# Optimization experiments

Measured on AMD Instinct MI355X. Metric: run time of the kernel, lower is better.

## Reference

```python
import jax, jax.numpy as jnp
import numpy as np

H, W = 72, 128            # raster_h, raster_w
THICK = 0.03              # raster_thickness
SHARP = 80.0              # sigmoid sharpness
NRS = 64                  # match_resample_n
BIG = 1e9                 # finite stand-in for inf (grad-safe)
PTS_W, TAN_W, CURV_W, OVL_W = 5.0, 1.0, 0.5, 2.0


def _grid_xy():
    ys = jnp.linspace(0.0, 1.0, H)
    xs = jnp.linspace(0.0, 1.0, W)
    yy, xx = jnp.meshgrid(ys, xs, indexing='ij')
    return jnp.stack([xx, yy], -1).reshape(-1, 2)  # [H*W, 2]


def _prepare_mask(vis):
    # visibility -> per-point mask; curves with <2 visible points fall back to all-visible
    raw = vis > 0.5
    fallback = raw.sum(-1) < 2
    return jnp.where(fallback[:, None], 1.0, raw.astype(jnp.float32))  # [m, p]


def _resample(curves, pm, num):
    # arc-length resampling of [m, p, 2] polylines to [m, num, 2]
    m, p, _ = curves.shape
    seg_valid = pm[:, :-1] * pm[:, 1:]
    seg_len = jnp.linalg.norm(curves[:, 1:] - curves[:, :-1], axis=-1) * seg_valid
    cum = jnp.concatenate([jnp.zeros((m, 1), curves.dtype), jnp.cumsum(seg_len, -1)], -1)  # [m, p]
    total = cum[:, -1]
    base_t = jnp.linspace(0.0, 1.0, num)
    t = base_t[None] * total[:, None]  # [m, num]
    idx = jax.vmap(lambda c, tt: jnp.searchsorted(c, tt, side='right'))(cum, t) - 1
    idx = jnp.clip(idx, 0, p - 2)
    left = jnp.take_along_axis(curves[:, :-1], idx[..., None], axis=1)
    right = jnp.take_along_axis(curves[:, 1:], idx[..., None], axis=1)
    lt = jnp.take_along_axis(cum[:, :-1], idx, axis=1)
    rt = jnp.take_along_axis(cum[:, 1:], idx, axis=1)
    alpha = ((t - lt) / jnp.maximum(rt - lt, 1e-8))[..., None]
    out = left + alpha * (right - left)
    return jnp.where((total < 1e-8)[:, None, None], curves[:, :1, :], out)


def _tangents(pts):
    # central-difference unit tangents, [m, n, 2]
    fwd = jnp.concatenate([pts[:, 1:2] - pts[:, 0:1],
                           pts[:, 2:] - pts[:, :-2],
                           pts[:, -1:] - pts[:, -2:-1]], axis=1)
    return fwd / jnp.maximum(jnp.linalg.norm(fwd, axis=-1, keepdims=True), 1e-8)


def _pt2poly(A, B):
    # mean over resampled points of A of min point-to-segment distance to polyline B
    # A: [qa, r, 2], B: [qb, r, 2] -> [qa, qb]
    seg_a = B[:, :-1]
    ab = B[:, 1:] - seg_a
    denom = jnp.maximum((ab * ab).sum(-1), 1e-8)  # [qb, s]
    ap = A[:, None, :, None, :] - seg_a[None, :, None]           # [qa, qb, r, s, 2]
    t = jnp.clip((ap * ab[None, :, None]).sum(-1) / denom[None, :, None], 0.0, 1.0)
    proj = seg_a[None, :, None] + t[..., None] * ab[None, :, None]
    dist = jnp.linalg.norm(A[:, None, :, None, :] - proj, axis=-1)  # [qa, qb, r, s]
    return dist.min(-1).mean(-1)


def _smooth_l1(x, y):
    d = jnp.abs(x - y)
    return jnp.where(d < 1.0, 0.5 * d * d, d - 0.5)


def _soft_mask(curves, pm, grid):
    # soft rasterization of polylines: [m, p, 2] -> [m, H*W]
    seg_a = curves[:, :-1]
    ab = curves[:, 1:] - seg_a
    denom = jnp.maximum((ab * ab).sum(-1), 1e-8)          # [m, s]
    seg_valid = (pm[:, :-1] * pm[:, 1:]) > 0.5
    ap = grid[None, :, None, :] - seg_a[:, None]          # [m, HW, s, 2]
    t = jnp.clip((ap * ab[:, None]).sum(-1) / denom[:, None], 0.0, 1.0)
    proj = seg_a[:, None] + t[..., None] * ab[:, None]
    dist = jnp.linalg.norm(grid[None, :, None, :] - proj, axis=-1)  # [m, HW, s]
    dist = jnp.where(seg_valid[:, None], dist, BIG)
    min_dist = dist.min(-1)
    # fallback to nearest visible point when a curve has no valid segment
    no_valid = ~seg_valid.any(-1)
    pd = jnp.linalg.norm(grid[None, :, None, :] - curves[:, None], axis=-1)  # [m, HW, p]
    pd = jnp.where(pm[:, None] > 0.5, pd, BIG)
    min_dist = jnp.where(no_valid[:, None], pd.min(-1), min_dist)
    return jax.nn.sigmoid((THICK - min_dist) * SHARP)


def _cost_single(pred, gtp, gtv, grid):
    gt_pm = _prepare_mask(gtv)
    ones_pm = jnp.ones(pred.shape[:2], pred.dtype)
    pred_rs = _resample(pred, ones_pm, NRS)
    gt_rs = _resample(gtp, gt_pm, NRS)
    d_pg = _pt2poly(pred_rs, gt_rs)
    d_gp = _pt2poly(gt_rs, pred_rs).T
    sym = 0.5 * (d_pg + d_gp)                                   # [Q, M]
    pt = _tangents(pred_rs)
    gt_t = _tangents(gt_rs)
    tan = 1.0 - jnp.abs((pt[:, None] * gt_t[None]).sum(-1)).mean(-1)
    ps = pred_rs[:, 2:] - 2 * pred_rs[:, 1:-1] + pred_rs[:, :-2]
    gs = gt_rs[:, 2:] - 2 * gt_rs[:, 1:-1] + gt_rs[:, :-2]
    curv = _smooth_l1(ps[:, None], gs[None]).mean((-1, -2))
    pmask = _soft_mask(pred, ones_pm, grid)                     # [Q, HW]
    gmask = _soft_mask(gtp, gt_pm, grid)                        # [M, HW]
    inter = jnp.minimum(pmask[:, None], gmask[None]).sum(-1)
    union = jnp.maximum(pmask[:, None], gmask[None]).sum(-1)
    overlap = 1.0 - inter / (union + 1e-8)
    return PTS_W * sym + TAN_W * tan + CURV_W * curv + OVL_W * overlap


def setup_inputs() -> dict:
    key = jax.random.key(0)
    k1, k2, k3, k4 = jax.random.split(key, 4)
    return {
        'pred_pts': jax.random.uniform(k1, (2, 40, 24, 2), jnp.float32),
        'gt_pts': jax.random.uniform(k2, (2, 24, 24, 2), jnp.float32),
        'gt_vis': jax.random.uniform(k3, (2, 24, 24), jnp.float32),
        'gt_exist': jax.random.uniform(k4, (2, 24), jnp.float32),
    }


def reference(pred_pts, gt_pts, gt_vis, gt_exist):
    grid = _grid_xy()
    cost = jax.vmap(lambda p, g, v: _cost_single(p, g, v, grid))(pred_pts, gt_pts, gt_vis)
    # zero out columns for non-existent GT lanes (original skips them via boolean indexing)
    return cost * (gt_exist > 0.5).astype(cost.dtype)[:, None, :]  # [B, Q, M]
```

## Files before the change

### kernel.cpp

```cpp
#include <hip/hip_runtime.h>
#include <math.h>

#define Hh 72
#define Ww 128
#define HW (Hh*Ww)
#define NP 24
#define NSEG (NP-1)
#define Mp 40
#define Ng 24
#define Bb 2
#define NRS 64
#define THICKc 0.03f
#define SHARPc 80.0f
#define NCURV (Bb*(Mp+Ng))

__global__ __launch_bounds__(64) void k_prep(
    const float* __restrict__ pred,
    const float* __restrict__ gt,
    const float* __restrict__ vis,
    float* __restrict__ predRS,
    float* __restrict__ gtRS,
    float* __restrict__ segData,
    int*   __restrict__ segCount)
{
    int c = blockIdx.x;
    bool isPred = (c < Bb * Mp);
    int b   = isPred ? (c / Mp) : ((c - Bb * Mp) / Ng);
    int idx = isPred ? (c % Mp) : ((c - Bb * Mp) % Ng);
    const float* src = isPred ? pred + (size_t)(b * Mp + idx) * NP * 2
                              : gt   + (size_t)(b * Ng + idx) * NP * 2;
    int tid = threadIdx.x;

    __shared__ float qx[NP], qy[NP], pm[NP], cum[NP];
    __shared__ int   sidx[NP];
    __shared__ int   s_mode;
    __shared__ float s_total;

    if (tid < NP) {
        float2 v = ((const float2*)src)[tid];
        qx[tid] = v.x; qy[tid] = v.y;
        pm[tid] = isPred ? 1.0f
                         : ((vis[(b * Ng + idx) * NP + tid] > 0.5f) ? 1.0f : 0.0f);
    }
    __syncthreads();
    if (tid == 0) {
        if (!isPred) {
            float s = 0.0f;
            for (int p = 0; p < NP; p++) s += pm[p];
            if (s < 2.0f)
                for (int p = 0; p < NP; p++) pm[p] = 1.0f;
        }
        float acc = 0.0f;
        cum[0] = 0.0f;
        for (int s = 0; s < NSEG; s++) {
            float dx = qx[s + 1] - qx[s], dy = qy[s + 1] - qy[s];
            acc += sqrtf(dx * dx + dy * dy) * (pm[s] * pm[s + 1]);
            cum[s + 1] = acc;
        }
        s_total = acc;
        int n = 0;
        for (int s = 0; s < NSEG; s++) sidx[s] = (pm[s] * pm[s + 1] > 0.5f) ? n++ : -1;
        if (n > 0) {
            s_mode = 0;
        } else {
            s_mode = 1;
            for (int p = 0; p < NP; p++) sidx[p] = (pm[p] > 0.5f) ? n++ : -1;
        }
        segCount[c] = n;
    }
    __syncthreads();

    if (s_mode == 0) {
        if (tid < NSEG && sidx[tid] >= 0) {
            float ax = qx[tid], ay = qy[tid];
            float abx = qx[tid + 1] - ax, aby = qy[tid + 1] - ay;
            float inv = 1.0f / fmaxf(abx * abx + aby * aby, 1e-8f);
            float* r = segData + ((size_t)c * NP + sidx[tid]) * 8;
            r[0] = ax;  r[1] = ay;  r[2] = abx;       r[3] = aby;
            r[4] = abx * inv; r[5] = aby * inv; r[6] = (ax * abx + ay * aby) * inv; r[7] = 0.f;
        }
    } else {
        if (tid < NP && sidx[tid] >= 0) {
            float* r = segData + ((size_t)c * NP + sidx[tid]) * 8;
            r[0] = qx[tid]; r[1] = qy[tid]; r[2] = 0.f; r[3] = 0.f;
            r[4] = 0.f;     r[5] = 0.f;     r[6] = 0.f; r[7] = 0.f;
        }
    }

    float total = s_total;
    float t = ((float)tid / 63.0f) * total;
    int cnt = 0;
    for (int p = 0; p < NP; p++) cnt += (cum[p] <= t) ? 1 : 0;
    int id2 = cnt - 1;
    id2 = (id2 < 0) ? 0 : ((id2 > NP - 2) ? NP - 2 : id2);
    float lt = cum[id2], rt = cum[id2 + 1];
    float alpha = (t - lt) / fmaxf(rt - lt, 1e-8f);
    float ox = qx[id2] + alpha * (qx[id2 + 1] - qx[id2]);
    float oy = qy[id2] + alpha * (qy[id2 + 1] - qy[id2]);
    if (total < 1e-8f) { ox = qx[0]; oy = qy[0]; }
    float* dst = isPred ? predRS + ((size_t)(b * Mp + idx) * NRS + tid) * 2
                        : gtRS   + ((size_t)(b * Ng + idx) * NRS + tid) * 2;
    dst[0] = ox; dst[1] = oy;
}

__global__ __launch_bounds__(256) void k_softmask(
    const float* __restrict__ segData,
    const int*   __restrict__ segCount,
    float* __restrict__ maskAll)
{
    int c = blockIdx.y;
    int g = blockIdx.x * 256 + threadIdx.x;
    int n = segCount[c];
    const float4* sd = (const float4*)(segData + (size_t)c * NP * 8);

    float gx = (float)(g & (Ww - 1)) * (1.0f / 127.0f);
    float gy = (float)(g >> 7)       * (1.0f / 71.0f);

    float best2 = 1e30f;
    for (int s = 0; s < n; s++) {
        float4 A  = sd[s * 2];
        float4 Bv = sd[s * 2 + 1];
        float t = fmaf(gx, Bv.x, fmaf(gy, Bv.y, -Bv.z));
        t = fminf(fmaxf(t, 0.0f), 1.0f);
        float dx = gx - fmaf(t, A.z, A.x);
        float dy = gy - fmaf(t, A.w, A.y);
        best2 = fminf(best2, fmaf(dx, dx, dy * dy));
    }
    float mind = sqrtf(best2);
    float mval = 1.0f / (1.0f + __expf((mind - THICKc) * SHARPc));
    maskAll[(size_t)c * HW + g] = mval;
}

__global__ __launch_bounds__(256) void k_cost(
    const float* __restrict__ predRS,
    const float* __restrict__ gtRS,
    const float* __restrict__ maskAll,
    const float* __restrict__ gtExist,
    float* __restrict__ out)
{
    int blk = blockIdx.x;
    int tj = blk % 12;
    int ti = (blk / 12) % 20;
    int b  = blk / (12 * 20);
    int i0 = ti * 2, j0 = tj * 2;
    int tid = threadIdx.x;
    int lane = tid & 63, w = tid >> 6;

    __shared__ float sPx[2][NRS], sPy[2][NRS], sGx[2][NRS], sGy[2][NRS];
    __shared__ float partA[4][8];
    __shared__ float cham[4][3];

    {
        int ci = tid >> 6, pt = tid & 63;
        if (ci < 2) {
            float2 v = ((const float2*)predRS)[(b * Mp + i0 + ci) * NRS + pt];
            sPx[ci][pt] = v.x; sPy[ci][pt] = v.y;
        } else {
            int cj = ci - 2;
            float2 v = ((const float2*)gtRS)[(b * Ng + j0 + cj) * NRS + pt];
            sGx[cj][pt] = v.x; sGy[cj][pt] = v.y;
        }
    }
    __syncthreads();

    const float4* P0 = (const float4*)(maskAll + (size_t)(b * Mp + i0)     * HW);
    const float4* P1 = (const float4*)(maskAll + (size_t)(b * Mp + i0 + 1) * HW);
    const float4* Q0 = (const float4*)(maskAll + (size_t)(Bb * Mp + b * Ng + j0)     * HW);
    const float4* Q1 = (const float4*)(maskAll + (size_t)(Bb * Mp + b * Ng + j0 + 1) * HW);
    float sm00 = 0, sm01 = 0, sm10 = 0, sm11 = 0;
    float sp0 = 0, sp1 = 0, sq0 = 0, sq1 = 0;
    for (int g = tid; g < HW / 4; g += 256) {
        float4 p0 = P0[g], p1 = P1[g], q0 = Q0[g], q1 = Q1[g];
        sp0 += p0.x + p0.y + p0.z + p0.w;
        sp1 += p1.x + p1.y + p1.z + p1.w;
        sq0 += q0.x + q0.y + q0.z + q0.w;
        sq1 += q1.x + q1.y + q1.z + q1.w;
        sm00 += fminf(p0.x,q0.x) + fminf(p0.y,q0.y) + fminf(p0.z,q0.z) + fminf(p0.w,q0.w);
        sm01 += fminf(p0.x,q1.x) + fminf(p0.y,q1.y) + fminf(p0.z,q1.z) + fminf(p0.w,q1.w);
        sm10 += fminf(p1.x,q0.x) + fminf(p1.y,q0.y) + fminf(p1.z,q0.z) + fminf(p1.w,q0.w);
        sm11 += fminf(p1.x,q1.x) + fminf(p1.y,q1.y) + fminf(p1.z,q1.z) + fminf(p1.w,q1.w);
    }
    for (int off = 32; off > 0; off >>= 1) {
        sm00 += __shfl_down(sm00, off); sm01 += __shfl_down(sm01, off);
        sm10 += __shfl_down(sm10, off); sm11 += __shfl_down(sm11, off);
        sp0  += __shfl_down(sp0,  off); sp1  += __shfl_down(sp1,  off);
        sq0  += __shfl_down(sq0,  off); sq1  += __shfl_down(sq1,  off);
    }
    if (lane == 0) {
        partA[w][0] = sm00; partA[w][1] = sm01; partA[w][2] = sm10; partA[w][3] = sm11;
        partA[w][4] = sp0;  partA[w][5] = sp1;  partA[w][6] = sq0;  partA[w][7] = sq1;
    }

    {
        int a = w >> 1, cj = w & 1;
        const float* PX = sPx[a];  const float* PY = sPy[a];
        const float* GX = sGx[cj]; const float* GY = sGy[cj];
        float p0x = PX[lane], p0y = PY[lane];
        float q0x = GX[lane], q0y = GY[lane];
        float b1 = 1e30f, b2 = 1e30f;
        for (int s = 0; s < NRS - 1; s++) {
            {
                float ax = GX[s], ay = GY[s];
                float abx = GX[s + 1] - ax, aby = GY[s + 1] - ay;
                float denom = fmaxf(abx * abx + aby * aby, 1e-8f);
                float t = ((p0x - ax) * abx + (p0y - ay) * aby) / denom;
                t = fminf(fmaxf(t, 0.0f), 1.0f);
                float dx = p0x - (ax + t * abx), dy = p0y - (ay + t * aby);
                b1 = fminf(b1, dx * dx + dy * dy);
            }
            {
                float ax = PX[s], ay = PY[s];
                float abx = PX[s + 1] - ax, aby = PY[s + 1] - ay;
                float denom = fmaxf(abx * abx + aby * aby, 1e-8f);
                float t = ((q0x - ax) * abx + (q0y - ay) * aby) / denom;
                t = fminf(fmaxf(t, 0.0f), 1.0f);
                float dx = q0x - (ax + t * abx), dy = q0y - (ay + t * aby);
                b2 = fminf(b2, dx * dx + dy * dy);
            }
        }
        float symv = 0.5f * (sqrtf(b1) + sqrtf(b2));

        int kp = (lane == NRS - 1) ? NRS - 1 : lane + 1;
        int km = (lane == 0) ? 0 : lane - 1;
        float tx = PX[kp] - PX[km], ty = PY[kp] - PY[km];
        float nrm = fmaxf(sqrtf(tx * tx + ty * ty), 1e-8f);
        tx /= nrm; ty /= nrm;
        float gtx = GX[kp] - GX[km], gty = GY[kp] - GY[km];
        float nrm2 = fmaxf(sqrtf(gtx * gtx + gty * gty), 1e-8f);
        gtx /= nrm2; gty /= nrm2;
        float tanv = fabsf(tx * gtx + ty * gty);

        float curvv = 0.0f;
        if (lane < NRS - 2) {
            float psx = PX[lane + 2] - 2.0f * PX[lane + 1] + PX[lane];
            float psy = PY[lane + 2] - 2.0f * PY[lane + 1] + PY[lane];
            float gsx = GX[lane + 2] - 2.0f * GX[lane + 1] + GX[lane];
            float gsy = GY[lane + 2] - 2.0f * GY[lane + 1] + GY[lane];
            float d1 = fabsf(psx - gsx);
            float d2 = fabsf(psy - gsy);
            float c1 = (d1 < 1.0f) ? 0.5f * d1 * d1 : d1 - 0.5f;
            float c2 = (d2 < 1.0f) ? 0.5f * d2 * d2 : d2 - 0.5f;
            curvv = c1 + c2;
        }
        for (int off = 32; off > 0; off >>= 1) {
            symv  += __shfl_down(symv,  off);
            tanv  += __shfl_down(tanv,  off);
            curvv += __shfl_down(curvv, off);
        }
        if (lane == 0) { cham[w][0] = symv; cham[w][1] = tanv; cham[w][2] = curvv; }
    }
    __syncthreads();

    if (tid < 4) {
        int a2 = tid >> 1, c2 = tid & 1;
        float Smin = partA[0][tid] + partA[1][tid] + partA[2][tid] + partA[3][tid];
        float Sp = partA[0][4 + a2] + partA[1][4 + a2] + partA[2][4 + a2] + partA[3][4 + a2];
        float Sq = partA[0][6 + c2] + partA[1][6 + c2] + partA[2][6 + c2] + partA[3][6 + c2];
        float Smax = Sp + Sq - Smin;
        float overlap = 1.0f - Smin / (Smax + 1e-8f);
        float sym  = cham[tid][0] * (1.0f / 64.0f);
        float tanl = 1.0f - cham[tid][1] * (1.0f / 64.0f);
        float curv = cham[tid][2] * (1.0f / 124.0f);
        float cost = 5.0f * sym + 1.0f * tanl + 0.5f * curv + 2.0f * overlap;
        float e = (gtExist[b * Ng + j0 + c2] > 0.5f) ? 1.0f : 0.0f;
        out[(size_t)(b * Mp + i0 + a2) * Ng + j0 + c2] = cost * e;
    }
}

extern "C" void kernel_launch(void* const* d_in, const int* in_sizes, int n_in,
                              void* d_out, int out_size, void* d_ws, size_t ws_size,
                              hipStream_t stream) {
    (void)in_sizes; (void)n_in; (void)out_size; (void)ws_size;
    const float* pred  = (const float*)d_in[0];
    const float* gt    = (const float*)d_in[1];
    const float* vis   = (const float*)d_in[2];
    const float* exist = (const float*)d_in[3];

    float* ws      = (float*)d_ws;
    float* predRS  = ws;
    float* gtRS    = predRS + (size_t)Bb * Mp * NRS * 2;
    float* segData = gtRS   + (size_t)Bb * Ng * NRS * 2;
    int*   segCount= (int*)(segData + (size_t)NCURV * NP * 8);
    float* maskAll = (float*)(segCount + 128);
    float* outp    = (float*)d_out;

    hipLaunchKernelGGL(k_prep, dim3(NCURV), dim3(64), 0, stream,
                       pred, gt, vis, predRS, gtRS, segData, segCount);
    hipLaunchKernelGGL(k_softmask, dim3(HW / 256, NCURV), dim3(256), 0, stream,
                       segData, segCount, maskAll);
    hipLaunchKernelGGL(k_cost, dim3(Bb * 20 * 12), dim3(256), 0, stream,
                       predRS, gtRS, maskAll, exist, outp);
}
```

Baseline: 100.8 us.

## Fuse three kernels into one cooperative kernel with grid-wide syncs

Merges the prep, soft-mask and cost kernels into a single cooperative launch of 480 blocks, with grid.sync barriers between the phases. The soft-mask phase becomes a grid-stride loop over curve and pixel-chunk tasks. The aim is to remove the launch gaps between three kernels. The cost is grid-barrier overhead, a fixed block count that must stay co-resident, and reduced parallelism in the mask phase.

Measured after the change: 312.9 us. 3.11x slower.

```diff
diff --git a/kernel.cpp b/kernel.cpp
--- a/kernel.cpp
+++ b/kernel.cpp
@@ -1,5 +1,8 @@
 #include <hip/hip_runtime.h>
+#include <hip/hip_cooperative_groups.h>
 #include <math.h>
+
+namespace cg = cooperative_groups;
 
 #define Hh 72
 #define Ww 128
@@ -13,22 +16,22 @@
 #define THICKc 0.03f
 #define SHARPc 80.0f
 #define NCURV (Bb*(Mp+Ng))
-
-__global__ __launch_bounds__(64) void k_prep(
+#define NBLK 480
+#define NCHUNK (HW/256)
+
+__global__ __launch_bounds__(256) void k_fused(
     const float* __restrict__ pred,
     const float* __restrict__ gt,
     const float* __restrict__ vis,
+    const float* __restrict__ gtExist,
     float* __restrict__ predRS,
     float* __restrict__ gtRS,
     float* __restrict__ segData,
-    int*   __restrict__ segCount)
+    int*   __restrict__ segCount,
+    float* __restrict__ maskAll,
+    float* __restrict__ out)
 {
-    int c = blockIdx.x;
-    bool isPred = (c < Bb * Mp);
-    int b   = isPred ? (c / Mp) : ((c - Bb * Mp) / Ng);
-    int idx = isPred ? (c % Mp) : ((c - Bb * Mp) % Ng);
-    const float* src = isPred ? pred + (size_t)(b * Mp + idx) * NP * 2
-                              : gt   + (size_t)(b * Ng + idx) * NP * 2;
+    cg::grid_group grid = cg::this_grid();
     int tid = threadIdx.x;
 
     __shared__ float qx[NP], qy[NP], pm[NP], cum[NP];
@@ -36,234 +39,237 @@
     __shared__ int   s_mode;
     __shared__ float s_total;
 
-    if (tid < NP) {
-        float2 v = ((const float2*)src)[tid];
-        qx[tid] = v.x; qy[tid] = v.y;
-        pm[tid] = isPred ? 1.0f
-                         : ((vis[(b * Ng + idx) * NP + tid] > 0.5f) ? 1.0f : 0.0f);
+    if (blockIdx.x < NCURV) {
+        int c = blockIdx.x;
+        bool isPred = (c < Bb * Mp);
+        int b   = isPred ? (c / Mp) : ((c - Bb * Mp) / Ng);
+        int idx = isPred ? (c % Mp) : ((c - Bb * Mp) % Ng);
+        const float* src = isPred ? pred + (size_t)(b * Mp + idx) * NP * 2
+                                  : gt   + (size_t)(b * Ng + idx) * NP * 2;
+        if (tid < NP) {
+            float2 v = ((const float2*)src)[tid];
+            qx[tid] = v.x; qy[tid] = v.y;
+            pm[tid] = isPred ? 1.0f
+                             : ((vis[(b * Ng + idx) * NP + tid] > 0.5f) ? 1.0f : 0.0f);
+        }
+        __syncthreads();
+        if (tid == 0) {
+            if (!isPred) {
+                float s = 0.0f;
+                for (int p = 0; p < NP; p++) s += pm[p];
+                if (s < 2.0f)
+                    for (int p = 0; p < NP; p++) pm[p] = 1.0f;
+            }
+            float acc = 0.0f;
+            cum[0] = 0.0f;
+            for (int s = 0; s < NSEG; s++) {
+                float dx = qx[s + 1] - qx[s], dy = qy[s + 1] - qy[s];
+                acc += sqrtf(dx * dx + dy * dy) * (pm[s] * pm[s + 1]);
+                cum[s + 1] = acc;
+            }
+            s_total = acc;
+            int n = 0;
+            for (int s = 0; s < NSEG; s++) sidx[s] = (pm[s] * pm[s + 1] > 0.5f) ? n++ : -1;
+            if (n > 0) {
+                s_mode = 0;
+            } else {
+                s_mode = 1;
+                for (int p = 0; p < NP; p++) sidx[p] = (pm[p] > 0.5f) ? n++ : -1;
+            }
+            segCount[c] = n;
+        }
+        __syncthreads();
+
+        if (s_mode == 0) {
+            if (tid < NSEG && sidx[tid] >= 0) {
+                float ax = qx[tid], ay = qy[tid];
+                float abx = qx[tid + 1] - ax, aby = qy[tid + 1] - ay;
+                float inv = 1.0f / fmaxf(abx * abx + aby * aby, 1e-8f);
+                float* r = segData + ((size_t)c * NP + sidx[tid]) * 8;
+                r[0] = ax;        r[1] = ay;        r[2] = abx; r[3] = aby;
+                r[4] = abx * inv; r[5] = aby * inv;
+                r[6] = (ax * abx + ay * aby) * inv; r[7] = 0.f;
+            }
+        } else {
+            if (tid < NP && sidx[tid] >= 0) {
+                float* r = segData + ((size_t)c * NP + sidx[tid]) * 8;
+                r[0] = qx[tid]; r[1] = qy[tid]; r[2] = 0.f; r[3] = 0.f;
+                r[4] = 0.f;     r[5] = 0.f;     r[6] = 0.f; r[7] = 0.f;
+            }
+        }
+
+        if (tid < NRS) {
+            float total = s_total;
+            float t = ((float)tid / 63.0f) * total;
+            int cnt = 0;
+            for (int p = 0; p < NP; p++) cnt += (cum[p] <= t) ? 1 : 0;
+            int id2 = cnt - 1;
+            id2 = (id2 < 0) ? 0 : ((id2 > NP - 2) ? NP - 2 : id2);
+            float lt = cum[id2], rt = cum[id2 + 1];
+            float alpha = (t - lt) / fmaxf(rt - lt, 1e-8f);
+            float ox = qx[id2] + alpha * (qx[id2 + 1] - qx[id2]);
+            float oy = qy[id2] + alpha * (qy[id2 + 1] - qy[id2]);
+            if (total < 1e-8f) { ox = qx[0]; oy = qy[0]; }
+            float* dst = isPred ? predRS + ((size_t)(b * Mp + idx) * NRS + tid) * 2
+                                : gtRS   + ((size_t)(b * Ng + idx) * NRS + tid) * 2;
+            dst[0] = ox; dst[1] = oy;
+        }
     }
-    __syncthreads();
-    if (tid == 0) {
-        if (!isPred) {
-            float s = 0.0f;
-            for (int p = 0; p < NP; p++) s += pm[p];
-            if (s < 2.0f)
-                for (int p = 0; p < NP; p++) pm[p] = 1.0f;
-        }
-        float acc = 0.0f;
-        cum[0] = 0.0f;
-        for (int s = 0; s < NSEG; s++) {
-            float dx = qx[s + 1] - qx[s], dy = qy[s + 1] - qy[s];
-            acc += sqrtf(dx * dx + dy * dy) * (pm[s] * pm[s + 1]);
-            cum[s + 1] = acc;
-        }
-        s_total = acc;
-        int n = 0;
-        for (int s = 0; s < NSEG; s++) sidx[s] = (pm[s] * pm[s + 1] > 0.5f) ? n++ : -1;
-        if (n > 0) {
-            s_mode = 0;
-        } else {
-            s_mode = 1;
-            for (int p = 0; p < NP; p++) sidx[p] = (pm[p] > 0.5f) ? n++ : -1;
-        }
-        segCount[c] = n;
+    __threadfence();
+    grid.sync();
+
+    for (int task = blockIdx.x; task < NCURV * NCHUNK; task += NBLK) {
+        int c = task / NCHUNK;
+        int g = (task % NCHUNK) * 256 + tid;
+        int n = segCount[c];
+        const float4* sd = (const float4*)(segData + (size_t)c * NP * 8);
+
+        float gx = (float)(g & (Ww - 1)) * (1.0f / 127.0f);
+        float gy = (float)(g >> 7)       * (1.0f / 71.0f);
+
+        float best2 = 1e30f;
+        for (int s = 0; s < n; s++) {
+            float4 A  = sd[s * 2];
+            float4 Bv = sd[s * 2 + 1];
+            float t = fmaf(gx, Bv.x, fmaf(gy, Bv.y, -Bv.z));
+            t = fminf(fmaxf(t, 0.0f), 1.0f);
+            float dx = gx - fmaf(t, A.z, A.x);
+            float dy = gy - fmaf(t, A.w, A.y);
+            best2 = fminf(best2, fmaf(dx, dx, dy * dy));
+        }
+        float mind = sqrtf(best2);
+        maskAll[(size_t)c * HW + g] = 1.0f / (1.0f + __expf((mind - THICKc) * SHARPc));
     }
-    __syncthreads();
-
-    if (s_mode == 0) {
-        if (tid < NSEG && sidx[tid] >= 0) {
-            float ax = qx[tid], ay = qy[tid];
-            float abx = qx[tid + 1] - ax, aby = qy[tid + 1] - ay;
-            float inv = 1.0f / fmaxf(abx * abx + aby * aby, 1e-8f);
-            float* r = segData + ((size_t)c * NP + sidx[tid]) * 8;
-            r[0] = ax;  r[1] = ay;  r[2] = abx;       r[3] = aby;
-            r[4] = abx * inv; r[5] = aby * inv; r[6] = (ax * abx + ay * aby) * inv; r[7] = 0.f;
-        }
-    } else {
-        if (tid < NP && sidx[tid] >= 0) {
-            float* r = segData + ((size_t)c * NP + sidx[tid]) * 8;
-            r[0] = qx[tid]; r[1] = qy[tid]; r[2] = 0.f; r[3] = 0.f;
-            r[4] = 0.f;     r[5] = 0.f;     r[6] = 0.f; r[7] = 0.f;
-        }
-    }
-
-    float total = s_total;
-    float t = ((float)tid / 63.0f) * total;
-    int cnt = 0;
-    for (int p = 0; p < NP; p++) cnt += (cum[p] <= t) ? 1 : 0;
-    int id2 = cnt - 1;
-    id2 = (id2 < 0) ? 0 : ((id2 > NP - 2) ? NP - 2 : id2);
-    float lt = cum[id2], rt = cum[id2 + 1];
-    float alpha = (t - lt) / fmaxf(rt - lt, 1e-8f);
-    float ox = qx[id2] + alpha * (qx[id2 + 1] - qx[id2]);
-    float oy = qy[id2] + alpha * (qy[id2 + 1] - qy[id2]);
-    if (total < 1e-8f) { ox = qx[0]; oy = qy[0]; }
-    float* dst = isPred ? predRS + ((size_t)(b * Mp + idx) * NRS + tid) * 2
-                        : gtRS   + ((size_t)(b * Ng + idx) * NRS + tid) * 2;
-    dst[0] = ox; dst[1] = oy;
-}
-
-__global__ __launch_bounds__(256) void k_softmask(
-    const float* __restrict__ segData,
-    const int*   __restrict__ segCount,
-    float* __restrict__ maskAll)
-{
-    int c = blockIdx.y;
-    int g = blockIdx.x * 256 + threadIdx.x;
-    int n = segCount[c];
-    const float4* sd = (const float4*)(segData + (size_t)c * NP * 8);
-
-    float gx = (float)(g & (Ww - 1)) * (1.0f / 127.0f);
-    float gy = (float)(g >> 7)       * (1.0f / 71.0f);
-
-    float best2 = 1e30f;
-    for (int s = 0; s < n; s++) {
-        float4 A  = sd[s * 2];
-        float4 Bv = sd[s * 2 + 1];
-        float t = fmaf(gx, Bv.x, fmaf(gy, Bv.y, -Bv.z));
-        t = fminf(fmaxf(t, 0.0f), 1.0f);
-        float dx = gx - fmaf(t, A.z, A.x);
-        float dy = gy - fmaf(t, A.w, A.y);
-        best2 = fminf(best2, fmaf(dx, dx, dy * dy));
-    }
-    float mind = sqrtf(best2);
-    float mval = 1.0f / (1.0f + __expf((mind - THICKc) * SHARPc));
-    maskAll[(size_t)c * HW + g] = mval;
-}
-
-__global__ __launch_bounds__(256) void k_cost(
-    const float* __restrict__ predRS,
-    const float* __restrict__ gtRS,
-    const float* __restrict__ maskAll,
-    const float* __restrict__ gtExist,
-    float* __restrict__ out)
-{
-    int blk = blockIdx.x;
-    int tj = blk % 12;
-    int ti = (blk / 12) % 20;
-    int b  = blk / (12 * 20);
-    int i0 = ti * 2, j0 = tj * 2;
-    int tid = threadIdx.x;
-    int lane = tid & 63, w = tid >> 6;
-
-    __shared__ float sPx[2][NRS], sPy[2][NRS], sGx[2][NRS], sGy[2][NRS];
-    __shared__ float partA[4][8];
-    __shared__ float cham[4][3];
+    __threadfence();
+    grid.sync();
 
     {
-        int ci = tid >> 6, pt = tid & 63;
-        if (ci < 2) {
-            float2 v = ((const float2*)predRS)[(b * Mp + i0 + ci) * NRS + pt];
-            sPx[ci][pt] = v.x; sPy[ci][pt] = v.y;
-        } else {
-            int cj = ci - 2;
-            float2 v = ((const float2*)gtRS)[(b * Ng + j0 + cj) * NRS + pt];
-            sGx[cj][pt] = v.x; sGy[cj][pt] = v.y;
-        }
-    }
-    __syncthreads();
-
-    const float4* P0 = (const float4*)(maskAll + (size_t)(b * Mp + i0)     * HW);
-    const float4* P1 = (const float4*)(maskAll + (size_t)(b * Mp + i0 + 1) * HW);
-    const float4* Q0 = (const float4*)(maskAll + (size_t)(Bb * Mp + b * Ng + j0)     * HW);
-    const float4* Q1 = (const float4*)(maskAll + (size_t)(Bb * Mp + b * Ng + j0 + 1) * HW);
-    float sm00 = 0, sm01 = 0, sm10 = 0, sm11 = 0;
-    float sp0 = 0, sp1 = 0, sq0 = 0, sq1 = 0;
-    for (int g = tid; g < HW / 4; g += 256) {
-        float4 p0 = P0[g], p1 = P1[g], q0 = Q0[g], q1 = Q1[g];
-        sp0 += p0.x + p0.y + p0.z + p0.w;
-        sp1 += p1.x + p1.y + p1.z + p1.w;
-        sq0 += q0.x + q0.y + q0.z + q0.w;
-        sq1 += q1.x + q1.y + q1.z + q1.w;
-        sm00 += fminf(p0.x,q0.x) + fminf(p0.y,q0.y) + fminf(p0.z,q0.z) + fminf(p0.w,q0.w);
-        sm01 += fminf(p0.x,q1.x) + fminf(p0.y,q1.y) + fminf(p0.z,q1.z) + fminf(p0.w,q1.w);
-        sm10 += fminf(p1.x,q0.x) + fminf(p1.y,q0.y) + fminf(p1.z,q0.z) + fminf(p1.w,q0.w);
-        sm11 += fminf(p1.x,q1.x) + fminf(p1.y,q1.y) + fminf(p1.z,q1.z) + fminf(p1.w,q1.w);
-    }
-    for (int off = 32; off > 0; off >>= 1) {
-        sm00 += __shfl_down(sm00, off); sm01 += __shfl_down(sm01, off);
-        sm10 += __shfl_down(sm10, off); sm11 += __shfl_down(sm11, off);
-        sp0  += __shfl_down(sp0,  off); sp1  += __shfl_down(sp1,  off);
-        sq0  += __shfl_down(sq0,  off); sq1  += __shfl_down(sq1,  off);
-    }
-    if (lane == 0) {
-        partA[w][0] = sm00; partA[w][1] = sm01; partA[w][2] = sm10; partA[w][3] = sm11;
-        partA[w][4] = sp0;  partA[w][5] = sp1;  partA[w][6] = sq0;  partA[w][7] = sq1;
-    }
-
-    {
-        int a = w >> 1, cj = w & 1;
-        const float* PX = sPx[a];  const float* PY = sPy[a];
-        const float* GX = sGx[cj]; const float* GY = sGy[cj];
-        float p0x = PX[lane], p0y = PY[lane];
-        float q0x = GX[lane], q0y = GY[lane];
-        float b1 = 1e30f, b2 = 1e30f;
-        for (int s = 0; s < NRS - 1; s++) {
-            {
-                float ax = GX[s], ay = GY[s];
-                float abx = GX[s + 1] - ax, aby = GY[s + 1] - ay;
-                float denom = fmaxf(abx * abx + aby * aby, 1e-8f);
-                float t = ((p0x - ax) * abx + (p0y - ay) * aby) / denom;
-                t = fminf(fmaxf(t, 0.0f), 1.0f);
-                float dx = p0x - (ax + t * abx), dy = p0y - (ay + t * aby);
-                b1 = fminf(b1, dx * dx + dy * dy);
-            }
-            {
-                float ax = PX[s], ay = PY[s];
-                float abx = PX[s + 1] - ax, aby = PY[s + 1] - ay;
-                float denom = fmaxf(abx * abx + aby * aby, 1e-8f);
-                float t = ((q0x - ax) * abx + (q0y - ay) * aby) / denom;
-                t = fminf(fmaxf(t, 0.0f), 1.0f);
-                float dx = q0x - (ax + t * abx), dy = q0y - (ay + t * aby);
-                b2 = fminf(b2, dx * dx + dy * dy);
-            }
-        }
-        float symv = 0.5f * (sqrtf(b1) + sqrtf(b2));
-
-        int kp = (lane == NRS - 1) ? NRS - 1 : lane + 1;
-        int km = (lane == 0) ? 0 : lane - 1;
-        float tx = PX[kp] - PX[km], ty = PY[kp] - PY[km];
-        float nrm = fmaxf(sqrtf(tx * tx + ty * ty), 1e-8f);
-        tx /= nrm; ty /= nrm;
-        float gtx = GX[kp] - GX[km], gty = GY[kp] - GY[km];
-        float nrm2 = fmaxf(sqrtf(gtx * gtx + gty * gty), 1e-8f);
-        gtx /= nrm2; gty /= nrm2;
-        float tanv = fabsf(tx * gtx + ty * gty);
-
-        float curvv = 0.0f;
-        if (lane < NRS - 2) {
-            float psx = PX[lane + 2] - 2.0f * PX[lane + 1] + PX[lane];
-            float psy = PY[lane + 2] - 2.0f * PY[lane + 1] + PY[lane];
-            float gsx = GX[lane + 2] - 2.0f * GX[lane + 1] + GX[lane];
-            float gsy = GY[lane + 2] - 2.0f * GY[lane + 1] + GY[lane];
-            float d1 = fabsf(psx - gsx);
-            float d2 = fabsf(psy - gsy);
-            float c1 = (d1 < 1.0f) ? 0.5f * d1 * d1 : d1 - 0.5f;
-            float c2 = (d2 < 1.0f) ? 0.5f * d2 * d2 : d2 - 0.5f;
-            curvv = c1 + c2;
+        int blk = blockIdx.x;
+        int tj = blk % 12;
+        int ti = (blk / 12) % 20;
+        int b  = blk / (12 * 20);
+        int i0 = ti * 2, j0 = tj * 2;
+        int lane = tid & 63, w = tid >> 6;
+
+        __shared__ float sPx[2][NRS], sPy[2][NRS], sGx[2][NRS], sGy[2][NRS];
+        __shared__ float partA[4][8];
+        __shared__ float cham[4][3];
+
+        {
+            int ci = tid >> 6, pt = tid & 63;
+            if (ci < 2) {
+                float2 v = ((const float2*)predRS)[(b * Mp + i0 + ci) * NRS + pt];
+                sPx[ci][pt] = v.x; sPy[ci][pt] = v.y;
+            } else {
+                int cj = ci - 2;
+                float2 v = ((const float2*)gtRS)[(b * Ng + j0 + cj) * NRS + pt];
+                sGx[cj][pt] = v.x; sGy[cj][pt] = v.y;
+            }
+        }
+        __syncthreads();
+
+        const float4* P0 = (const float4*)(maskAll + (size_t)(b * Mp + i0)     * HW);
+        const float4* P1 = (const float4*)(maskAll + (size_t)(b * Mp + i0 + 1) * HW);
+        const float4* Q0 = (const float4*)(maskAll + (size_t)(Bb * Mp + b * Ng + j0)     * HW);
+        const float4* Q1 = (const float4*)(maskAll + (size_t)(Bb * Mp + b * Ng + j0 + 1) * HW);
+        float sm00 = 0, sm01 = 0, sm10 = 0, sm11 = 0;
+        float sp0 = 0, sp1 = 0, sq0 = 0, sq1 = 0;
+        for (int g = tid; g < HW / 4; g += 256) {
+            float4 p0 = P0[g], p1 = P1[g], q0 = Q0[g], q1 = Q1[g];
+            sp0 += p0.x + p0.y + p0.z + p0.w;
+            sp1 += p1.x + p1.y + p1.z + p1.w;
+            sq0 += q0.x + q0.y + q0.z + q0.w;
+            sq1 += q1.x + q1.y + q1.z + q1.w;
+            sm00 += fminf(p0.x,q0.x) + fminf(p0.y,q0.y) + fminf(p0.z,q0.z) + fminf(p0.w,q0.w);
+            sm01 += fminf(p0.x,q1.x) + fminf(p0.y,q1.y) + fminf(p0.z,q1.z) + fminf(p0.w,q1.w);
+            sm10 += fminf(p1.x,q0.x) + fminf(p1.y,q0.y) + fminf(p1.z,q0.z) + fminf(p1.w,q0.w);
+            sm11 += fminf(p1.x,q1.x) + fminf(p1.y,q1.y) + fminf(p1.z,q1.z) + fminf(p1.w,q1.w);
         }
         for (int off = 32; off > 0; off >>= 1) {
-            symv  += __shfl_down(symv,  off);
-            tanv  += __shfl_down(tanv,  off);
-            curvv += __shfl_down(curvv, off);
-        }
-        if (lane == 0) { cham[w][0] = symv; cham[w][1] = tanv; cham[w][2] = curvv; }
-    }
-    __syncthreads();
-
-    if (tid < 4) {
-        int a2 = tid >> 1, c2 = tid & 1;
-        float Smin = partA[0][tid] + partA[1][tid] + partA[2][tid] + partA[3][tid];
-        float Sp = partA[0][4 + a2] + partA[1][4 + a2] + partA[2][4 + a2] + partA[3][4 + a2];
-        float Sq = partA[0][6 + c2] + partA[1][6 + c2] + partA[2][6 + c2] + partA[3][6 + c2];
-        float Smax = Sp + Sq - Smin;
-        float overlap = 1.0f - Smin / (Smax + 1e-8f);
-        float sym  = cham[tid][0] * (1.0f / 64.0f);
-        float tanl = 1.0f - cham[tid][1] * (1.0f / 64.0f);
-        float curv = cham[tid][2] * (1.0f / 124.0f);
-        float cost = 5.0f * sym + 1.0f * tanl + 0.5f * curv + 2.0f * overlap;
-        float e = (gtExist[b * Ng + j0 + c2] > 0.5f) ? 1.0f : 0.0f;
-        out[(size_t)(b * Mp + i0 + a2) * Ng + j0 + c2] = cost * e;
+            sm00 += __shfl_down(sm00, off); sm01 += __shfl_down(sm01, off);
+            sm10 += __shfl_down(sm10, off); sm11 += __shfl_down(sm11, off);
+            sp0  += __shfl_down(sp0,  off); sp1  += __shfl_down(sp1,  off);
+            sq0  += __shfl_down(sq0,  off); sq1  += __shfl_down(sq1,  off);
+        }
+        if (lane == 0) {
+            partA[w][0] = sm00; partA[w][1] = sm01; partA[w][2] = sm10; partA[w][3] = sm11;
+            partA[w][4] = sp0;  partA[w][5] = sp1;  partA[w][6] = sq0;  partA[w][7] = sq1;
+        }
+
+        {
+            int a = w >> 1, cj = w & 1;
+            const float* PX = sPx[a];  const float* PY = sPy[a];
+            const float* GX = sGx[cj]; const float* GY = sGy[cj];
+            float p0x = PX[lane], p0y = PY[lane];
+            float q0x = GX[lane], q0y = GY[lane];
+            float b1 = 1e30f, b2 = 1e30f;
+            for (int s = 0; s < NRS - 1; s++) {
+                {
+                    float ax = GX[s], ay = GY[s];
+                    float abx = GX[s + 1] - ax, aby = GY[s + 1] - ay;
+                    float denom = fmaxf(abx * abx + aby * aby, 1e-8f);
+                    float t = ((p0x - ax) * abx + (p0y - ay) * aby) / denom;
+                    t = fminf(fmaxf(t, 0.0f), 1.0f);
+                    float dx = p0x - (ax + t * abx), dy = p0y - (ay + t * aby);
+                    b1 = fminf(b1, dx * dx + dy * dy);
+                }
+                {
+                    float ax = PX[s], ay = PY[s];
+                    float abx = PX[s + 1] - ax, aby = PY[s + 1] - ay;
+                    float denom = fmaxf(abx * abx + aby * aby, 1e-8f);
+                    float t = ((q0x - ax) * abx + (q0y - ay) * aby) / denom;
+                    t = fminf(fmaxf(t, 0.0f), 1.0f);
+                    float dx = q0x - (ax + t * abx), dy = q0y - (ay + t * aby);
+                    b2 = fminf(b2, dx * dx + dy * dy);
+                }
+            }
+            float symv = 0.5f * (sqrtf(b1) + sqrtf(b2));
+
+            int kp = (lane == NRS - 1) ? NRS - 1 : lane + 1;
+            int km = (lane == 0) ? 0 : lane - 1;
+            float tx = PX[kp] - PX[km], ty = PY[kp] - PY[km];
+            float nrm = fmaxf(sqrtf(tx * tx + ty * ty), 1e-8f);
+            tx /= nrm; ty /= nrm;
+            float gtx = GX[kp] - GX[km], gty = GY[kp] - GY[km];
+            float nrm2 = fmaxf(sqrtf(gtx * gtx + gty * gty), 1e-8f);
+            gtx /= nrm2; gty /= nrm2;
+            float tanv = fabsf(tx * gtx + ty * gty);
+
+            float curvv = 0.0f;
+            if (lane < NRS - 2) {
+                float psx = PX[lane + 2] - 2.0f * PX[lane + 1] + PX[lane];
+                float psy = PY[lane + 2] - 2.0f * PY[lane + 1] + PY[lane];
+                float gsx = GX[lane + 2] - 2.0f * GX[lane + 1] + GX[lane];
+                float gsy = GY[lane + 2] - 2.0f * GY[lane + 1] + GY[lane];
+                float d1 = fabsf(psx - gsx);
+                float d2 = fabsf(psy - gsy);
+                float c1 = (d1 < 1.0f) ? 0.5f * d1 * d1 : d1 - 0.5f;
+                float c2 = (d2 < 1.0f) ? 0.5f * d2 * d2 : d2 - 0.5f;
+                curvv = c1 + c2;
+            }
+            for (int off = 32; off > 0; off >>= 1) {
+                symv  += __shfl_down(symv,  off);
+                tanv  += __shfl_down(tanv,  off);
+                curvv += __shfl_down(curvv, off);
+            }
+            if (lane == 0) { cham[w][0] = symv; cham[w][1] = tanv; cham[w][2] = curvv; }
+        }
+        __syncthreads();
+
+        if (tid < 4) {
+            int a2 = tid >> 1, c2 = tid & 1;
+            float Smin = partA[0][tid] + partA[1][tid] + partA[2][tid] + partA[3][tid];
+            float Sp = partA[0][4 + a2] + partA[1][4 + a2] + partA[2][4 + a2] + partA[3][4 + a2];
+            float Sq = partA[0][6 + c2] + partA[1][6 + c2] + partA[2][6 + c2] + partA[3][6 + c2];
+            float Smax = Sp + Sq - Smin;
+            float overlap = 1.0f - Smin / (Smax + 1e-8f);
+            float sym  = cham[tid][0] * (1.0f / 64.0f);
+            float tanl = 1.0f - cham[tid][1] * (1.0f / 64.0f);
+            float curv = cham[tid][2] * (1.0f / 124.0f);
+            float cost = 5.0f * sym + 1.0f * tanl + 0.5f * curv + 2.0f * overlap;
+            float e = (gtExist[b * Ng + j0 + c2] > 0.5f) ? 1.0f : 0.0f;
+            out[(size_t)(b * Mp + i0 + a2) * Ng + j0 + c2] = cost * e;
+        }
     }
 }
 
@@ -284,10 +290,9 @@
     float* maskAll = (float*)(segCount + 128);
     float* outp    = (float*)d_out;
 
-    hipLaunchKernelGGL(k_prep, dim3(NCURV), dim3(64), 0, stream,
-                       pred, gt, vis, predRS, gtRS, segData, segCount);
-    hipLaunchKernelGGL(k_softmask, dim3(HW / 256, NCURV), dim3(256), 0, stream,
-                       segData, segCount, maskAll);
-    hipLaunchKernelGGL(k_cost, dim3(Bb * 20 * 12), dim3(256), 0, stream,
-                       predRS, gtRS, maskAll, exist, outp);
+    void* args[] = { (void*)&pred, (void*)&gt, (void*)&vis, (void*)&exist,
+                     (void*)&predRS, (void*)&gtRS, (void*)&segData,
+                     (void*)&segCount, (void*)&maskAll, (void*)&outp };
+    hipLaunchCooperativeKernel((void*)k_fused, dim3(NBLK), dim3(256),
+                               args, 0, stream);
 }
```
